# Kernel tuning notes

Measured on AMD Instinct MI355X. Metric: run time of the kernel, lower is better.

## Reference

```python
import jax, jax.numpy as jnp
import numpy as np

D_MODEL = 2048
D_STATE = 16
BATCH = 2048

def setup_inputs() -> dict:
    key = jax.random.key(0)
    ks = jax.random.split(key, 8)
    x_t = jax.random.normal(ks[0], (BATCH, D_MODEL), dtype=jnp.float32)
    ssm_state_prev = jax.random.normal(ks[1], (BATCH, D_MODEL, D_STATE), dtype=jnp.float32)
    # parameters (match torch init semantics loosely; values random)
    A_log = jnp.log(jnp.tile(jnp.arange(1, D_STATE + 1, dtype=jnp.float32)[None, :], (D_MODEL, 1)))
    s = 1.0 / np.sqrt(D_MODEL)
    W_B = jax.random.uniform(ks[2], (D_STATE, D_MODEL), minval=-s, maxval=s, dtype=jnp.float32)
    W_C = jax.random.uniform(ks[3], (D_STATE, D_MODEL), minval=-s, maxval=s, dtype=jnp.float32)
    W_Delta = jax.random.uniform(ks[4], (D_MODEL, D_MODEL), minval=-s, maxval=s, dtype=jnp.float32)
    b_Delta = jax.random.uniform(ks[5], (D_MODEL,), minval=-s, maxval=s, dtype=jnp.float32)
    D_param = jnp.ones((D_MODEL,), dtype=jnp.float32)
    return {"x_t": x_t, "ssm_state_prev": ssm_state_prev, "A_log": A_log,
            "W_B": W_B, "W_C": W_C, "W_Delta": W_Delta, "b_Delta": b_Delta,
            "D_param": D_param}

def reference(x_t, ssm_state_prev, A_log, W_B, W_C, W_Delta, b_Delta, D_param):
    A = -jnp.exp(A_log)                         # (d_model, d_state)
    B_t = x_t @ W_B.T                            # (B, d_state)
    C_t = x_t @ W_C.T                            # (B, d_state)
    Delta_t = jax.nn.softplus(x_t @ W_Delta.T + b_Delta)   # (B, d_model)
    A_bar = jnp.exp(Delta_t[:, :, None] * A[None, :, :])   # (B, d_model, d_state)
    Delta_B = Delta_t[:, :, None] * B_t[:, None, :]         # (B, d_model, d_state)
    ssm_state_t = A_bar * ssm_state_prev + Delta_B * x_t[:, :, None]
    y_t = jnp.sum(ssm_state_t * C_t[:, None, :], axis=-1) + D_param * x_t
    return (y_t, ssm_state_t)
```

## Files before the change

### kernel.cpp

```cpp
#include <hip/hip_runtime.h>

#define D_MODEL 2048
#define D_STATE 16
#define BATCH   2048

typedef __attribute__((ext_vector_type(8))) short bf16x8;
typedef __attribute__((ext_vector_type(4))) float f32x4;
typedef __attribute__((ext_vector_type(8))) unsigned short u16x8;

__device__ __forceinline__ unsigned short f2bf(float f) {
  unsigned u = __float_as_uint(f);
  u = (u + 0x7FFFu + ((u >> 16) & 1u)) >> 16;
  return (unsigned short)u;
}

__device__ __forceinline__ void cvt8(const float* __restrict__ s, unsigned short* __restrict__ d) {
  float4 a = *(const float4*)s;
  float4 b = *(const float4*)(s + 4);
  u16x8 o;
  o[0] = f2bf(a.x); o[1] = f2bf(a.y); o[2] = f2bf(a.z); o[3] = f2bf(a.w);
  o[4] = f2bf(b.x); o[5] = f2bf(b.y); o[6] = f2bf(b.z); o[7] = f2bf(b.w);
  *(u16x8*)d = o;
}

__global__ __launch_bounds__(256) void prep_kernel(
    const float* __restrict__ x, const float* __restrict__ wd,
    const float* __restrict__ wb, const float* __restrict__ wc,
    unsigned short* __restrict__ x_bf, unsigned short* __restrict__ w_bf,
    unsigned short* __restrict__ wbc) {
  int t = blockIdx.x * 256 + threadIdx.x;
  if (t < 524288) {
    int base = t * 8;
    cvt8(x + base, x_bf + base);
  } else if (t < 1048576) {
    int base = (t - 524288) * 8;
    cvt8(wd + base, w_bf + base);
  } else {
    int i = (t - 1048576) * 8;
    int row = i >> 11, col = i & 2047;
    if (row < 16)      cvt8(wb + row * 2048 + col, wbc + i);
    else if (row < 32) cvt8(wc + (row - 16) * 2048 + col, wbc + i);
    else { u16x8 z = {0,0,0,0,0,0,0,0}; *(u16x8*)(wbc + i) = z; }
  }
}

__global__ __launch_bounds__(256) void gemm_kernel(
    const unsigned short* __restrict__ Abf,
    const unsigned short* __restrict__ Wbf,
    const unsigned short* __restrict__ WBC,
    const float* __restrict__ bias,
    float* __restrict__ Delta,
    float* __restrict__ BC) {
  __shared__ __align__(16) unsigned short lA[128 * 32];
  __shared__ __align__(16) unsigned short lB[128 * 32];

  const int tid = threadIdx.x;
  const bool isBC = (blockIdx.y == 16);
  const int brow = blockIdx.x * 128;
  const int bcol = isBC ? 0 : blockIdx.y * 128;
  const unsigned short* Bsrc = isBC ? WBC : (Wbf + (size_t)bcol * 2048);
  const unsigned short* Asrc = Abf + (size_t)brow * 2048;

  const int r0 = (tid * 16) >> 6;
  const int c0 = ((tid * 16) & 63) >> 1;
  const int ldsbase = (tid >> 6) << 10;

  const int lane = tid & 63;
  const int wid = tid >> 6;
  const int wr = wid >> 1, wcid = wid & 1;
  const int fr = lane & 15;
  const int kg = lane >> 4;

  f32x4 acc[4][4];
#pragma unroll
  for (int m = 0; m < 4; ++m)
#pragma unroll
    for (int n = 0; n < 4; ++n) acc[m][n] = (f32x4){0.f, 0.f, 0.f, 0.f};

  for (int k0 = 0; k0 < 2048; k0 += 32) {
    __syncthreads();
#pragma unroll
    for (int i = 0; i < 2; ++i) {
      const unsigned short* ga = Asrc + (size_t)(r0 + i * 64) * 2048 + k0 + c0;
      __builtin_amdgcn_global_load_lds(
          (const __attribute__((address_space(1))) void*)ga,
          (__attribute__((address_space(3))) void*)((char*)lA + i * 4096 + ldsbase),
          16, 0, 0);
      const unsigned short* gb = Bsrc + (size_t)(r0 + i * 64) * 2048 + k0 + c0;
      __builtin_amdgcn_global_load_lds(
          (const __attribute__((address_space(1))) void*)gb,
          (__attribute__((address_space(3))) void*)((char*)lB + i * 4096 + ldsbase),
          16, 0, 0);
    }
    __syncthreads();

    bf16x8 fa[4], fb[4];
#pragma unroll
    for (int m = 0; m < 4; ++m) {
      int row = wr * 64 + m * 16 + fr;
      fa[m] = *(const bf16x8*)&lA[row * 32 + kg * 8];
    }
#pragma unroll
    for (int n = 0; n < 4; ++n) {
      int col = wcid * 64 + n * 16 + fr;
      fb[n] = *(const bf16x8*)&lB[col * 32 + kg * 8];
    }
#pragma unroll
    for (int m = 0; m < 4; ++m)
#pragma unroll
      for (int n = 0; n < 4; ++n)
        acc[m][n] = __builtin_amdgcn_mfma_f32_16x16x32_bf16(fa[m], fb[n], acc[m][n], 0, 0, 0);
  }

  const int rq = kg * 4;
#pragma unroll
  for (int m = 0; m < 4; ++m) {
    int grow = brow + wr * 64 + m * 16 + rq;
#pragma unroll
    for (int n = 0; n < 4; ++n) {
      int gcol = bcol + wcid * 64 + n * 16 + fr;
      if (!isBC) {
        float bv = bias[gcol];
#pragma unroll
        for (int q = 0; q < 4; ++q) {
          float v = acc[m][n][q] + bv;
          v = fmaxf(v, 0.f) + log1pf(__expf(-fabsf(v)));
          Delta[(size_t)(grow + q) * 2048 + gcol] = v;
        }
      } else {
#pragma unroll
        for (int q = 0; q < 4; ++q)
          BC[(size_t)(grow + q) * 128 + gcol] = acc[m][n][q];
      }
    }
  }
}

__global__ __launch_bounds__(256) void pointwise_kernel(
    const float* __restrict__ x, const float* __restrict__ sp,
    const float* __restrict__ A_log, const float* __restrict__ BCb,
    const float* __restrict__ Delta, const float* __restrict__ Dp,
    float* __restrict__ y, float* __restrict__ st) {
  int t = blockIdx.x * 256 + threadIdx.x;
  int sg = t & 3;
  int d = (t >> 2) & 2047;
  int b = t >> 13;
  int bd = (b << 11) + d;
  float delta = Delta[bd];
  float xv = x[bd];
  float4 spv = ((const float4*)sp)[t];
  float4 al  = ((const float4*)A_log)[(d << 2) + sg];
  float4 bt  = ((const float4*)BCb)[(b << 5) + sg];
  float4 ct  = ((const float4*)BCb)[(b << 5) + 4 + sg];
  float dx = delta * xv;
  float4 s;
  s.x = __expf(-delta * __expf(al.x)) * spv.x + dx * bt.x;
  s.y = __expf(-delta * __expf(al.y)) * spv.y + dx * bt.y;
  s.z = __expf(-delta * __expf(al.z)) * spv.z + dx * bt.z;
  s.w = __expf(-delta * __expf(al.w)) * spv.w + dx * bt.w;
  ((float4*)st)[t] = s;
  float p = s.x * ct.x + s.y * ct.y + s.z * ct.z + s.w * ct.w;
  p += __shfl_xor(p, 1, 4);
  p += __shfl_xor(p, 2, 4);
  if (sg == 0) y[bd] = p + Dp[d] * xv;
}

extern "C" void kernel_launch(void* const* d_in, const int* in_sizes, int n_in,
                              void* d_out, int out_size, void* d_ws, size_t ws_size,
                              hipStream_t stream) {
  const float* x    = (const float*)d_in[0];
  const float* sp   = (const float*)d_in[1];
  const float* alog = (const float*)d_in[2];
  const float* wb   = (const float*)d_in[3];
  const float* wc   = (const float*)d_in[4];
  const float* wd   = (const float*)d_in[5];
  const float* bdel = (const float*)d_in[6];
  const float* dp   = (const float*)d_in[7];
  float* y  = (float*)d_out;
  float* st = (float*)d_out + (size_t)BATCH * D_MODEL;

  char* ws = (char*)d_ws;
  unsigned short* x_bf = (unsigned short*)ws;
  unsigned short* w_bf = (unsigned short*)(ws + 8388608);
  unsigned short* wbc  = (unsigned short*)(ws + 16777216);
  float* Delta = (float*)(ws + 17301504);
  float* BC    = (float*)(ws + 34078720);

  prep_kernel<<<4224, 256, 0, stream>>>(x, wd, wb, wc, x_bf, w_bf, wbc);
  gemm_kernel<<<dim3(16, 17), 256, 0, stream>>>(x_bf, w_bf, wbc, bdel, Delta, BC);
  pointwise_kernel<<<65536, 256, 0, stream>>>(x, sp, alog, BC, Delta, dp, y, st);
}
```

Baseline: 539.2 us.

## Double-buffer GEMM with swizzled LDS, precompute exp(A_log), widen pointwise per thread

The GEMM now uses two LDS buffers with a K-tile of 64. It prefetches the next tile while computing the current one and applies an XOR swizzle to avoid LDS bank conflicts. The prep kernel additionally precomputes exp(A_log), so the pointwise kernel drops one exp per state element. The pointwise kernel also handles 8 state elements per thread using nontemporal loads and stores. This doubles LDS use and adds register pressure in the GEMM. The pointwise change mainly trims instruction count in a kernel that is likely bandwidth-bound.

```diff
diff --git a/kernel.cpp b/kernel.cpp
--- a/kernel.cpp
+++ b/kernel.cpp
@@ -15,32 +15,38 @@
 }
 
 __device__ __forceinline__ void cvt8(const float* __restrict__ s, unsigned short* __restrict__ d) {
-  float4 a = *(const float4*)s;
-  float4 b = *(const float4*)(s + 4);
+  f32x4 a = *(const f32x4*)s;
+  f32x4 b = *(const f32x4*)(s + 4);
   u16x8 o;
-  o[0] = f2bf(a.x); o[1] = f2bf(a.y); o[2] = f2bf(a.z); o[3] = f2bf(a.w);
-  o[4] = f2bf(b.x); o[5] = f2bf(b.y); o[6] = f2bf(b.z); o[7] = f2bf(b.w);
+  o[0] = f2bf(a[0]); o[1] = f2bf(a[1]); o[2] = f2bf(a[2]); o[3] = f2bf(a[3]);
+  o[4] = f2bf(b[0]); o[5] = f2bf(b[1]); o[6] = f2bf(b[2]); o[7] = f2bf(b[3]);
   *(u16x8*)d = o;
 }
 
 __global__ __launch_bounds__(256) void prep_kernel(
     const float* __restrict__ x, const float* __restrict__ wd,
     const float* __restrict__ wb, const float* __restrict__ wc,
+    const float* __restrict__ alog,
     unsigned short* __restrict__ x_bf, unsigned short* __restrict__ w_bf,
-    unsigned short* __restrict__ wbc) {
+    unsigned short* __restrict__ wbc, float* __restrict__ nA) {
   int t = blockIdx.x * 256 + threadIdx.x;
   if (t < 524288) {
-    int base = t * 8;
-    cvt8(x + base, x_bf + base);
+    cvt8(x + t * 8, x_bf + t * 8);
   } else if (t < 1048576) {
-    int base = (t - 524288) * 8;
-    cvt8(wd + base, w_bf + base);
-  } else {
+    int i = (t - 524288) * 8;
+    cvt8(wd + i, w_bf + i);
+  } else if (t < 1081344) {
     int i = (t - 1048576) * 8;
     int row = i >> 11, col = i & 2047;
     if (row < 16)      cvt8(wb + row * 2048 + col, wbc + i);
     else if (row < 32) cvt8(wc + (row - 16) * 2048 + col, wbc + i);
     else { u16x8 z = {0,0,0,0,0,0,0,0}; *(u16x8*)(wbc + i) = z; }
+  } else {
+    int i = (t - 1081344) * 4;
+    f32x4 v = *(const f32x4*)(alog + i);
+    f32x4 o;
+    o[0] = __expf(v[0]); o[1] = __expf(v[1]); o[2] = __expf(v[2]); o[3] = __expf(v[3]);
+    *(f32x4*)(nA + i) = o;
   }
 }
 
@@ -51,8 +57,8 @@
     const float* __restrict__ bias,
     float* __restrict__ Delta,
     float* __restrict__ BC) {
-  __shared__ __align__(16) unsigned short lA[128 * 32];
-  __shared__ __align__(16) unsigned short lB[128 * 32];
+  __shared__ __align__(16) unsigned short lA[2][8192];
+  __shared__ __align__(16) unsigned short lB[2][8192];
 
   const int tid = threadIdx.x;
   const bool isBC = (blockIdx.y == 16);
@@ -61,56 +67,82 @@
   const unsigned short* Bsrc = isBC ? WBC : (Wbf + (size_t)bcol * 2048);
   const unsigned short* Asrc = Abf + (size_t)brow * 2048;
 
-  const int r0 = (tid * 16) >> 6;
-  const int c0 = ((tid * 16) & 63) >> 1;
-  const int ldsbase = (tid >> 6) << 10;
-
   const int lane = tid & 63;
   const int wid = tid >> 6;
   const int wr = wid >> 1, wcid = wid & 1;
   const int fr = lane & 15;
   const int kg = lane >> 4;
 
+  int srcoff[4];
+#pragma unroll
+  for (int i = 0; i < 4; ++i) {
+    int ci = i * 256 + tid;
+    int r = ci >> 3, cs = ci & 7;
+    int c = cs ^ (r & 7);
+    srcoff[i] = r * 2048 + c * 8;
+  }
+  const int ldsb = (tid >> 6) << 10;
+
   f32x4 acc[4][4];
 #pragma unroll
   for (int m = 0; m < 4; ++m)
 #pragma unroll
     for (int n = 0; n < 4; ++n) acc[m][n] = (f32x4){0.f, 0.f, 0.f, 0.f};
 
-  for (int k0 = 0; k0 < 2048; k0 += 32) {
-    __syncthreads();
-#pragma unroll
-    for (int i = 0; i < 2; ++i) {
-      const unsigned short* ga = Asrc + (size_t)(r0 + i * 64) * 2048 + k0 + c0;
-      __builtin_amdgcn_global_load_lds(
-          (const __attribute__((address_space(1))) void*)ga,
-          (__attribute__((address_space(3))) void*)((char*)lA + i * 4096 + ldsbase),
-          16, 0, 0);
-      const unsigned short* gb = Bsrc + (size_t)(r0 + i * 64) * 2048 + k0 + c0;
-      __builtin_amdgcn_global_load_lds(
-          (const __attribute__((address_space(1))) void*)gb,
-          (__attribute__((address_space(3))) void*)((char*)lB + i * 4096 + ldsbase),
-          16, 0, 0);
-    }
-    __syncthreads();
-
-    bf16x8 fa[4], fb[4];
+#define STAGE(buf, k0)                                                          \
+  do {                                                                          \
+    _Pragma("unroll")                                                           \
+    for (int i = 0; i < 4; ++i)                                                 \
+      __builtin_amdgcn_global_load_lds(                                         \
+          (const __attribute__((address_space(1))) void*)(Asrc + (size_t)srcoff[i] + (k0)), \
+          (__attribute__((address_space(3))) void*)((char*)lA[buf] + i * 4096 + ldsb), \
+          16, 0, 0);                                                            \
+    _Pragma("unroll")                                                           \
+    for (int i = 0; i < 4; ++i)                                                 \
+      __builtin_amdgcn_global_load_lds(                                         \
+          (const __attribute__((address_space(1))) void*)(Bsrc + (size_t)srcoff[i] + (k0)), \
+          (__attribute__((address_space(3))) void*)((char*)lB[buf] + i * 4096 + ldsb), \
+          16, 0, 0);                                                            \
+  } while (0)
+
+  STAGE(0, 0);
+  asm volatile("s_waitcnt vmcnt(0)" ::: "memory");
+  __builtin_amdgcn_s_barrier();
+  int cur = 0;
+#pragma unroll 1
+  for (int t = 0; t < 32; ++t) {
+    if (t < 31) STAGE(cur ^ 1, (t + 1) * 64);
+
+    bf16x8 fa[2][4], fb[2][4];
 #pragma unroll
     for (int m = 0; m < 4; ++m) {
       int row = wr * 64 + m * 16 + fr;
-      fa[m] = *(const bf16x8*)&lA[row * 32 + kg * 8];
+#pragma unroll
+      for (int kk = 0; kk < 2; ++kk)
+        fa[kk][m] = *(const bf16x8*)((const char*)lA[cur] + row * 128 +
+                                     ((((kk << 2) + kg) ^ (row & 7)) << 4));
     }
 #pragma unroll
     for (int n = 0; n < 4; ++n) {
-      int col = wcid * 64 + n * 16 + fr;
-      fb[n] = *(const bf16x8*)&lB[col * 32 + kg * 8];
+      int row = wcid * 64 + n * 16 + fr;
+#pragma unroll
+      for (int kk = 0; kk < 2; ++kk)
+        fb[kk][n] = *(const bf16x8*)((const char*)lB[cur] + row * 128 +
+                                     ((((kk << 2) + kg) ^ (row & 7)) << 4));
     }
 #pragma unroll
-    for (int m = 0; m < 4; ++m)
-#pragma unroll
-      for (int n = 0; n < 4; ++n)
-        acc[m][n] = __builtin_amdgcn_mfma_f32_16x16x32_bf16(fa[m], fb[n], acc[m][n], 0, 0, 0);
-  }
+    for (int kk = 0; kk < 2; ++kk)
+#pragma unroll
+      for (int m = 0; m < 4; ++m)
+#pragma unroll
+        for (int n = 0; n < 4; ++n)
+          acc[m][n] = __builtin_amdgcn_mfma_f32_16x16x32_bf16(fa[kk][m], fb[kk][n], acc[m][n], 0, 0, 0);
+
+    asm volatile("s_waitcnt vmcnt(0)" ::: "memory");
+    __builtin_amdgcn_s_barrier();
+    cur ^= 1;
+  }
+#undef STAGE
 
   const int rq = kg * 4;
 #pragma unroll
@@ -138,30 +170,40 @@
 
 __global__ __launch_bounds__(256) void pointwise_kernel(
     const float* __restrict__ x, const float* __restrict__ sp,
-    const float* __restrict__ A_log, const float* __restrict__ BCb,
+    const float* __restrict__ nA, const float* __restrict__ BCb,
     const float* __restrict__ Delta, const float* __restrict__ Dp,
     float* __restrict__ y, float* __restrict__ st) {
   int t = blockIdx.x * 256 + threadIdx.x;
-  int sg = t & 3;
-  int d = (t >> 2) & 2047;
-  int b = t >> 13;
+  int sg = t & 1;
+  int d = (t >> 1) & 2047;
+  int b = t >> 12;
   int bd = (b << 11) + d;
   float delta = Delta[bd];
   float xv = x[bd];
-  float4 spv = ((const float4*)sp)[t];
-  float4 al  = ((const float4*)A_log)[(d << 2) + sg];
-  float4 bt  = ((const float4*)BCb)[(b << 5) + sg];
-  float4 ct  = ((const float4*)BCb)[(b << 5) + 4 + sg];
   float dx = delta * xv;
-  float4 s;
-  s.x = __expf(-delta * __expf(al.x)) * spv.x + dx * bt.x;
-  s.y = __expf(-delta * __expf(al.y)) * spv.y + dx * bt.y;
-  s.z = __expf(-delta * __expf(al.z)) * spv.z + dx * bt.z;
-  s.w = __expf(-delta * __expf(al.w)) * spv.w + dx * bt.w;
-  ((float4*)st)[t] = s;
-  float p = s.x * ct.x + s.y * ct.y + s.z * ct.z + s.w * ct.w;
-  p += __shfl_xor(p, 1, 4);
-  p += __shfl_xor(p, 2, 4);
+  const f32x4* spp = (const f32x4*)sp + ((size_t)t << 1);
+  f32x4 s0 = __builtin_nontemporal_load(spp);
+  f32x4 s1 = __builtin_nontemporal_load(spp + 1);
+  const f32x4* ap = (const f32x4*)nA + ((d << 2) + (sg << 1));
+  f32x4 a0 = ap[0], a1 = ap[1];
+  const f32x4* bp = (const f32x4*)BCb + ((b << 5) + (sg << 1));
+  f32x4 b0 = bp[0], b1 = bp[1];
+  f32x4 c0 = bp[4], c1 = bp[5];
+  f32x4 r0, r1;
+  r0[0] = __expf(-delta * a0[0]) * s0[0] + dx * b0[0];
+  r0[1] = __expf(-delta * a0[1]) * s0[1] + dx * b0[1];
+  r0[2] = __expf(-delta * a0[2]) * s0[2] + dx * b0[2];
+  r0[3] = __expf(-delta * a0[3]) * s0[3] + dx * b0[3];
+  r1[0] = __expf(-delta * a1[0]) * s1[0] + dx * b1[0];
+  r1[1] = __expf(-delta * a1[1]) * s1[1] + dx * b1[1];
+  r1[2] = __expf(-delta * a1[2]) * s1[2] + dx * b1[2];
+  r1[3] = __expf(-delta * a1[3]) * s1[3] + dx * b1[3];
+  f32x4* stp = (f32x4*)st + ((size_t)t << 1);
+  __builtin_nontemporal_store(r0, stp);
+  __builtin_nontemporal_store(r1, stp + 1);
+  float p = r0[0] * c0[0] + r0[1] * c0[1] + r0[2] * c0[2] + r0[3] * c0[3]
+          + r1[0] * c1[0] + r1[1] * c1[1] + r1[2] * c1[2] + r1[3] * c1[3];
+  p += __shfl_xor(p, 1, 2);
   if (sg == 0) y[bd] = p + Dp[d] * xv;
 }
 
@@ -185,8 +227,9 @@
   unsigned short* wbc  = (unsigned short*)(ws + 16777216);
   float* Delta = (float*)(ws + 17301504);
   float* BC    = (float*)(ws + 34078720);
-
-  prep_kernel<<<4224, 256, 0, stream>>>(x, wd, wb, wc, x_bf, w_bf, wbc);
+  float* nA    = (float*)(ws + 35127296);
+
+  prep_kernel<<<4256, 256, 0, stream>>>(x, wd, wb, wc, alog, x_bf, w_bf, wbc, nA);
   gemm_kernel<<<dim3(16, 17), 256, 0, stream>>>(x_bf, w_bf, wbc, bdel, Delta, BC);
-  pointwise_kernel<<<65536, 256, 0, stream>>>(x, sp, alog, BC, Delta, dp, y, st);
-}
+  pointwise_kernel<<<32768, 256, 0, stream>>>(x, sp, nA, BC, Delta, dp, y, st);
+}
```

New measurement: 547.4 us. No clear change (+1.5%).
